# Performance work log

Measured on AMD Instinct MI355X. Metric: run time of the kernel, lower is better.

The kernel has to match this reference:

```python
import jax, jax.numpy as jnp
import numpy as np

B, C, H, W = 16, 384, 128, 128
RED = 6                      # reduction
CH = C // RED                # 64
CF = C // 2 + 1              # 193 rfft bins


def setup_inputs() -> dict:
    key = jax.random.key(0)
    ks = jax.random.split(key, 9)
    sc = 0.05
    return {
        "x":   jax.random.normal(ks[0], (B, C, H, W), dtype=jnp.float32),
        "W1":  jax.random.normal(ks[1], (CH, C, 3, 3), dtype=jnp.float32) * sc,
        "b1":  jax.random.normal(ks[2], (CH,), dtype=jnp.float32) * sc,
        "W2":  jax.random.normal(ks[3], (C, CH, 3, 3), dtype=jnp.float32) * sc,
        "b2":  jax.random.normal(ks[4], (C,), dtype=jnp.float32) * sc,
        "Ws1": jax.random.normal(ks[5], (CF, C), dtype=jnp.float32) * sc,
        "bs1": jax.random.normal(ks[6], (CF,), dtype=jnp.float32) * sc,
        "Ws2": jax.random.normal(ks[7], (CF, C), dtype=jnp.float32) * sc,
        "bs2": jax.random.normal(ks[8], (CF,), dtype=jnp.float32) * sc,
    }


def reference(x, W1, b1, W2, b2, Ws1, bs1, Ws2, bs2):
    b, c = x.shape[0], x.shape[1]
    # global average pool -> [b, c]
    y0 = jnp.mean(x, axis=(2, 3))
    # fc: 3x3 convs on 1x1 spatial input (pad=1) reduce to center-tap matmuls
    h = jax.nn.relu(y0 @ W1[:, :, 1, 1].T + b1)            # [b, c//red]
    y = jax.nn.sigmoid(h @ W2[:, :, 1, 1].T + b2)          # [b, c]
    # seq1 / seq2: 1x1 convs on [b, c, 1, 1]
    s1 = jax.nn.relu(y @ Ws1.T + bs1)                      # [b, c//2+1]
    s2 = jax.nn.relu(y @ Ws2.T + bs2)                      # [b, c//2+1]
    # rfft2 over (1, c) spatial dims == 1-D rfft over channel axis
    yf = jnp.fft.rfft(y, axis=-1)                          # [b, c//2+1] complex
    amp = jnp.abs(yf) * s1
    pha = jnp.angle(yf) * s2
    rec = jax.lax.complex(amp * jnp.cos(pha), amp * jnp.sin(pha))
    xr = jnp.fft.irfft(rec, n=c, axis=-1)                  # [b, c]
    out = (xr * y)[:, :, None, None]                       # [b, c, 1, 1]
    return out
```

## Files before the change

kernel.cpp:

```cpp
#include <hip/hip_runtime.h>

#define BB 16
#define CC 384
#define CH 64
#define CF 193
#define HW 16384

__global__ __launch_bounds__(256) void pool_kernel(const float4* __restrict__ x,
                                                   float* __restrict__ y0) {
    const int plane = blockIdx.x;
    const float4* p = x + (size_t)plane * (HW / 4);
    const int t = threadIdx.x;

    float s = 0.f;
#pragma unroll
    for (int r = 0; r < HW / 4 / 256; ++r) {
        float4 v = p[t + 256 * r];
        s += v.x + v.y + v.z + v.w;
    }

#pragma unroll
    for (int off = 32; off > 0; off >>= 1) s += __shfl_down(s, off);

    __shared__ float red[4];
    const int wid = t >> 6, lane = t & 63;
    if (lane == 0) red[wid] = s;
    __syncthreads();
    if (t == 0) {
        float tot = red[0] + red[1] + red[2] + red[3];
        y0[plane] = tot * (1.0f / (float)HW);
    }
}

__global__ __launch_bounds__(384) void head_kernel(
    const float* __restrict__ y0g,
    const float* __restrict__ W1,  const float* __restrict__ b1,
    const float* __restrict__ W2,  const float* __restrict__ b2,
    const float* __restrict__ Ws1, const float* __restrict__ bs1,
    const float* __restrict__ Ws2, const float* __restrict__ bs2,
    float* __restrict__ out)
{
    __shared__ float y0[CC], h[CH], y[CC];
    __shared__ float ct[CC], st[CC];
    __shared__ float rr[CF], ri[CF];

    const int b = blockIdx.x, t = threadIdx.x;

    y0[t] = y0g[b * CC + t];
    {
        float ang = (float)t * (6.283185307179586f / (float)CC);
        float sv, cv;
        sincosf(ang, &sv, &cv);
        st[t] = sv; ct[t] = cv;
    }
    __syncthreads();

    if (t < CH) {
        float acc = b1[t];
        const float* w = W1 + (size_t)t * CC * 9 + 4;
        for (int c = 0; c < CC; ++c) acc += y0[c] * w[c * 9];
        h[t] = fmaxf(acc, 0.f);
    }
    __syncthreads();

    {
        float acc = b2[t];
        const float* w = W2 + (size_t)t * CH * 9 + 4;
        for (int j = 0; j < CH; ++j) acc += h[j] * w[j * 9];
        y[t] = 1.f / (1.f + expf(-acc));
    }
    __syncthreads();

    if (t < CF) {
        const float* w1r = Ws1 + (size_t)t * CC;
        const float* w2r = Ws2 + (size_t)t * CC;
        float a1 = bs1[t], a2 = bs2[t];
        float re = 0.f, im = 0.f;
        int m = 0;
        for (int c = 0; c < CC; ++c) {
            float yc = y[c];
            a1 += yc * w1r[c];
            a2 += yc * w2r[c];
            re += yc * ct[m];
            im -= yc * st[m];
            m += t; if (m >= CC) m -= CC;
        }
        a1 = fmaxf(a1, 0.f);
        a2 = fmaxf(a2, 0.f);
        float amp = sqrtf(re * re + im * im) * a1;
        float pha = atan2f(im, re) * a2;
        float sp, cp;
        sincosf(pha, &sp, &cp);
        rr[t] = amp * cp;
        ri[t] = amp * sp;
    }
    __syncthreads();

    {
        float acc = 0.f;
        int m = 0;
        for (int k = 1; k < 192; ++k) {
            m += t; if (m >= CC) m -= CC;
            acc += rr[k] * ct[m] - ri[k] * st[m];
        }
        float nyq = (t & 1) ? -rr[192] : rr[192];
        float xr = (rr[0] + 2.f * acc + nyq) * (1.0f / (float)CC);
        out[b * CC + t] = xr * y[t];
    }
}

extern "C" void kernel_launch(void* const* d_in, const int* in_sizes, int n_in,
                              void* d_out, int out_size, void* d_ws, size_t ws_size,
                              hipStream_t stream) {
    const float4* x = (const float4*)d_in[0];
    const float* W1  = (const float*)d_in[1];
    const float* b1  = (const float*)d_in[2];
    const float* W2  = (const float*)d_in[3];
    const float* b2  = (const float*)d_in[4];
    const float* Ws1 = (const float*)d_in[5];
    const float* bs1 = (const float*)d_in[6];
    const float* Ws2 = (const float*)d_in[7];
    const float* bs2 = (const float*)d_in[8];
    float* out = (float*)d_out;

    float* y0 = (float*)d_ws;

    pool_kernel<<<BB * CC, 256, 0, stream>>>(x, y0);
    head_kernel<<<BB, 384, 0, stream>>>(y0, W1, b1, W2, b2, Ws1, bs1, Ws2, bs2, out);
}
```

Measured before the change: 615.8 us.

## Parallelize head-kernel matvecs across all threads with split-K and wave reductions

The first FC layer is split across six 64-channel partial sums so all 384 threads work, with partials combined through shared memory. The seq1/seq2 matvecs and the DFT are reassigned so each wavefront handles one frequency bin, with lanes striding over channels for coalesced weight loads, followed by shuffle reductions. This targets the latency of the single-block-per-batch head kernel, where few threads walked long serial loops with strided loads. The pool kernel, which likely dominates total time, is unchanged.

```diff
diff --git a/kernel.cpp b/kernel.cpp
--- a/kernel.cpp
+++ b/kernel.cpp
@@ -42,9 +42,12 @@
 {
     __shared__ float y0[CC], h[CH], y[CC];
     __shared__ float ct[CC], st[CC];
-    __shared__ float rr[CF], ri[CF];
+    __shared__ float rr[CF + 1], ri[CF + 1];
+    __shared__ float reS[CF], imS[CF], a1S[CF], a2S[CF];
+    __shared__ float hp[6][CH];
 
     const int b = blockIdx.x, t = threadIdx.x;
+    const int wid = t >> 6, lane = t & 63;
 
     y0[t] = y0g[b * CC + t];
     {
@@ -55,10 +58,19 @@
     }
     __syncthreads();
 
+    {
+        const int j = t & 63, part = t >> 6;
+        const float* w  = W1 + ((size_t)j * CC + part * 64) * 9 + 4;
+        const float* yy = y0 + part * 64;
+        float acc = 0.f;
+#pragma unroll 8
+        for (int c = 0; c < 64; ++c) acc += yy[c] * w[c * 9];
+        hp[part][j] = acc;
+    }
+    __syncthreads();
     if (t < CH) {
-        float acc = b1[t];
-        const float* w = W1 + (size_t)t * CC * 9 + 4;
-        for (int c = 0; c < CC; ++c) acc += y0[c] * w[c * 9];
+        float acc = b1[t] + hp[0][t] + hp[1][t] + hp[2][t]
+                          + hp[3][t] + hp[4][t] + hp[5][t];
         h[t] = fmaxf(acc, 0.f);
     }
     __syncthreads();
@@ -66,27 +78,43 @@
     {
         float acc = b2[t];
         const float* w = W2 + (size_t)t * CH * 9 + 4;
+#pragma unroll 8
         for (int j = 0; j < CH; ++j) acc += h[j] * w[j * 9];
         y[t] = 1.f / (1.f + expf(-acc));
     }
     __syncthreads();
 
-    if (t < CF) {
-        const float* w1r = Ws1 + (size_t)t * CC;
-        const float* w2r = Ws2 + (size_t)t * CC;
-        float a1 = bs1[t], a2 = bs2[t];
-        float re = 0.f, im = 0.f;
-        int m = 0;
-        for (int c = 0; c < CC; ++c) {
+    for (int k = wid; k < CF; k += 6) {
+        const float* w1r = Ws1 + (size_t)k * CC;
+        const float* w2r = Ws2 + (size_t)k * CC;
+        int m   = (k * lane) % CC;
+        int inc = (k << 6) % CC;
+        float a1 = 0.f, a2 = 0.f, re = 0.f, im = 0.f;
+#pragma unroll
+        for (int i = 0; i < 6; ++i) {
+            const int c = lane + (i << 6);
             float yc = y[c];
             a1 += yc * w1r[c];
             a2 += yc * w2r[c];
             re += yc * ct[m];
             im -= yc * st[m];
-            m += t; if (m >= CC) m -= CC;
+            m += inc; if (m >= CC) m -= CC;
         }
-        a1 = fmaxf(a1, 0.f);
-        a2 = fmaxf(a2, 0.f);
+#pragma unroll
+        for (int off = 32; off > 0; off >>= 1) {
+            a1 += __shfl_down(a1, off);
+            a2 += __shfl_down(a2, off);
+            re += __shfl_down(re, off);
+            im += __shfl_down(im, off);
+        }
+        if (lane == 0) { a1S[k] = a1; a2S[k] = a2; reS[k] = re; imS[k] = im; }
+    }
+    __syncthreads();
+
+    if (t < CF) {
+        float a1 = fmaxf(a1S[t] + bs1[t], 0.f);
+        float a2 = fmaxf(a2S[t] + bs2[t], 0.f);
+        float re = reS[t], im = imS[t];
         float amp = sqrtf(re * re + im * im) * a1;
         float pha = atan2f(im, re) * a2;
         float sp, cp;
```

New measurement: 600.0 us. -2.6%, faster.
